# Optimization experiments

Measured on AMD Instinct MI355X. Metric: run time of the kernel, lower is better.

Reference implementation:

```python
import jax, jax.numpy as jnp
import numpy as np

D_MODEL = 1024
N_HEADS = 16
D_HEAD = D_MODEL // N_HEADS


def setup_inputs() -> dict:
    key = jax.random.key(0)
    k1, k2, k3, k4, k5 = jax.random.split(key, 5)
    B, S = 2, 2048
    scale_in = 1.0 / np.sqrt(D_MODEL)
    return {
        "x": jax.random.normal(k1, (B, S, D_MODEL), dtype=jnp.float32),
        "qkv_w": jax.random.normal(k2, (3 * D_MODEL, D_MODEL), dtype=jnp.float32) * scale_in,
        "qkv_b": jax.random.normal(k3, (3 * D_MODEL,), dtype=jnp.float32) * 0.02,
        "out_w": jax.random.normal(k4, (D_MODEL, D_MODEL), dtype=jnp.float32) * scale_in,
        "out_b": jax.random.normal(k5, (D_MODEL,), dtype=jnp.float32) * 0.02,
    }


def reference(x, qkv_w, qkv_b, out_w, out_b) -> jnp.ndarray:
    B, S, D = x.shape
    # qkv projection: torch Linear stores weight as (out, in)
    qkv = x @ qkv_w.T + qkv_b                      # [B,S,3D]
    qkv = qkv.reshape(B, S, 3, N_HEADS, D_HEAD)
    qkv = jnp.transpose(qkv, (2, 0, 3, 1, 4))      # [3,B,H,S,d]
    q, k, v = qkv[0], qkv[1], qkv[2]
    scale = 1.0 / np.sqrt(D_HEAD).astype(np.float32)
    scores = jnp.einsum("bhsd,bhtd->bhst", q, k) * scale  # [B,H,S,S]
    attn = jax.nn.softmax(scores, axis=-1)
    out = jnp.einsum("bhst,bhtd->bhsd", attn, v)   # [B,H,S,d]
    out = jnp.transpose(out, (0, 2, 1, 3)).reshape(B, S, D)
    return out @ out_w.T + out_b
```

## Files before the change

### kernel.cpp

```cpp
#include <hip/hip_runtime.h>

typedef __bf16 bf16;
typedef __bf16 bf16x4 __attribute__((ext_vector_type(4)));
typedef __bf16 bf16x8 __attribute__((ext_vector_type(8)));
typedef float  f32x4  __attribute__((ext_vector_type(4)));

__device__ __forceinline__ void gld16(const void* g, void* l) {
  __builtin_amdgcn_global_load_lds(
      (const __attribute__((address_space(1))) void*)g,
      (__attribute__((address_space(3))) void*)l, 16, 0, 0);
}

__global__ void f2bf4_kernel(const float* __restrict__ in, bf16* __restrict__ out, int n4) {
  int i = blockIdx.x * blockDim.x + threadIdx.x;
  if (i < n4) {
    float4 v = reinterpret_cast<const float4*>(in)[i];
    bf16x4 o = { (bf16)v.x, (bf16)v.y, (bf16)v.z, (bf16)v.w };
    reinterpret_cast<bf16x4*>(out)[i] = o;
  }
}

template<int MODE>
__global__ __launch_bounds__(256)
void gemm_bt(const bf16* __restrict__ A, const bf16* __restrict__ B,
             const float* __restrict__ bias, void* __restrict__ Cout,
             int K, int N) {
  __shared__ bf16 As[128 * 64];
  __shared__ bf16 Bs[128 * 64];
  const int tid  = threadIdx.x;
  const int wave = tid >> 6, lane = tid & 63;
  const int quad = lane >> 4, l16 = lane & 15;
  const int bm = blockIdx.x * 128, bn = blockIdx.y * 128;
  const int wr = (wave >> 1) * 64, wc = (wave & 1) * 64;
  const int arow = lane >> 3;
  const int acol = (lane & 7) * 8;

  f32x4 acc[4][4] = {};

  const bf16* Ab = A + (size_t)bm * K;
  const bf16* Bb = B + (size_t)bn * K;

  for (int k0 = 0; k0 < K; k0 += 64) {
#pragma unroll
    for (int i = 0; i < 4; ++i) {
      int c = wave * 4 + i;
      gld16(Ab + (size_t)(c * 8 + arow) * K + k0 + acol, As + c * 512);
      gld16(Bb + (size_t)(c * 8 + arow) * K + k0 + acol, Bs + c * 512);
    }
    __syncthreads();
#pragma unroll
    for (int kk = 0; kk < 64; kk += 32) {
      bf16x8 af[4], bfr[4];
#pragma unroll
      for (int i = 0; i < 4; ++i)
        af[i]  = *(const bf16x8*)(As + (wr + i * 16 + l16) * 64 + kk + quad * 8);
#pragma unroll
      for (int i = 0; i < 4; ++i)
        bfr[i] = *(const bf16x8*)(Bs + (wc + i * 16 + l16) * 64 + kk + quad * 8);
#pragma unroll
      for (int i = 0; i < 4; ++i)
#pragma unroll
        for (int j = 0; j < 4; ++j)
          acc[i][j] = __builtin_amdgcn_mfma_f32_16x16x32_bf16(af[i], bfr[j], acc[i][j], 0, 0, 0);
    }
    __syncthreads();
  }

  if constexpr (MODE == 0) {
    bf16* Q = (bf16*)Cout;
#pragma unroll
    for (int j = 0; j < 4; ++j) {
      int col = bn + wc + j * 16 + l16;
      float bv  = bias[col];
      int sec = col >> 10, rem = col & 1023;
      int h = rem >> 6, d = rem & 63;
      float scl = (sec == 0) ? 0.125f * 1.44269504f : 1.0f;
#pragma unroll
      for (int i = 0; i < 4; ++i) {
#pragma unroll
        for (int r = 0; r < 4; ++r) {
          int row = bm + wr + i * 16 + quad * 4 + r;
          int b = row >> 11, si = row & 2047;
          float v = (acc[i][j][r] + bv) * scl;
          Q[(((size_t)sec * 32 + b * 16 + h) * 2048 + si) * 64 + d] = (bf16)v;
        }
      }
    }
  } else {
    float* C = (float*)Cout;
#pragma unroll
    for (int j = 0; j < 4; ++j) {
      int col = bn + wc + j * 16 + l16;
      float bv = bias[col];
#pragma unroll
      for (int i = 0; i < 4; ++i)
#pragma unroll
        for (int r = 0; r < 4; ++r) {
          int row = bm + wr + i * 16 + quad * 4 + r;
          C[(size_t)row * N + col] = acc[i][j][r] + bv;
        }
    }
  }
}

__global__ __launch_bounds__(256)
void transpose_v(const bf16* __restrict__ V, bf16* __restrict__ Vt) {
  __shared__ bf16 t[64][72];
  int bh = blockIdx.y, s0 = blockIdx.x * 64;
  const bf16* Vb = V + ((size_t)bh * 2048 + s0) * 64;
  bf16* Vtb = Vt + (size_t)bh * 64 * 2048 + s0;
  int tid = threadIdx.x;
#pragma unroll
  for (int p = 0; p < 2; ++p) {
    int r = p * 32 + (tid >> 3), c0 = (tid & 7) * 8;
    bf16x8 v = *(const bf16x8*)(Vb + r * 64 + c0);
#pragma unroll
    for (int j = 0; j < 8; ++j) t[c0 + j][r] = v[j];
  }
  __syncthreads();
#pragma unroll
  for (int p = 0; p < 2; ++p) {
    int d = p * 32 + (tid >> 3), s = (tid & 7) * 8;
    *(bf16x8*)(Vtb + (size_t)d * 2048 + s) = *(const bf16x8*)(&t[d][s]);
  }
}

__global__ __launch_bounds__(256, 2)
void attn_kernel(const bf16* __restrict__ QKV, const bf16* __restrict__ Vt,
                 bf16* __restrict__ O) {
  __shared__ bf16 Qs[128 * 72];
  __shared__ bf16 Ks[128 * 72];
  __shared__ bf16 Ps[4][32 * 144];

  const int bh = blockIdx.y;
  const int q0 = blockIdx.x * 128;
  const bf16* Qg = QKV + ((size_t)bh * 2048 + q0) * 64;
  const bf16* Kg = QKV + (size_t)32 * 2048 * 64 + (size_t)bh * 2048 * 64;
  const bf16* Vg = Vt + (size_t)bh * 64 * 2048;

  const int tid  = threadIdx.x;
  const int wave = tid >> 6, lane = tid & 63;
  const int quad = lane >> 4, l16 = lane & 15;
  const int srow = tid >> 3;
  const int scol = (tid & 7) * 8;

#pragma unroll
  for (int ch = 0; ch < 4; ++ch) {
    int row = ch * 32 + srow;
    *(bf16x8*)(Qs + row * 72 + scol) = *(const bf16x8*)(Qg + row * 64 + scol);
  }

  float rs[2][4] = {};
  f32x4 o[2][4] = {};

  for (int kt = 0; kt < 16; ++kt) {
    bf16x8 kreg[4];
#pragma unroll
    for (int ch = 0; ch < 4; ++ch)
      kreg[ch] = *(const bf16x8*)(Kg + (size_t)(kt * 128 + ch * 32 + srow) * 64 + scol);

    bf16x8 bv[4][4];
#pragma unroll
    for (int kk = 0; kk < 4; ++kk)
#pragma unroll
      for (int oj = 0; oj < 4; ++oj)
        bv[kk][oj] = *(const bf16x8*)(Vg + (size_t)(oj * 16 + l16) * 2048 +
                                      kt * 128 + kk * 32 + quad * 8);

    __syncthreads();
#pragma unroll
    for (int ch = 0; ch < 4; ++ch)
      *(bf16x8*)(Ks + (ch * 32 + srow) * 72 + scol) = kreg[ch];
    __syncthreads();

    f32x4 s[2][8] = {};
#pragma unroll
    for (int kk = 0; kk < 64; kk += 32) {
      bf16x8 aq0 = *(const bf16x8*)(Qs + (wave * 32 + l16) * 72 + kk + quad * 8);
      bf16x8 aq1 = *(const bf16x8*)(Qs + (wave * 32 + 16 + l16) * 72 + kk + quad * 8);
#pragma unroll
      for (int ni = 0; ni < 8; ++ni) {
        bf16x8 bk = *(const bf16x8*)(Ks + (ni * 16 + l16) * 72 + kk + quad * 8);
        s[0][ni] = __builtin_amdgcn_mfma_f32_16x16x32_bf16(aq0, bk, s[0][ni], 0, 0, 0);
        s[1][ni] = __builtin_amdgcn_mfma_f32_16x16x32_bf16(aq1, bk, s[1][ni], 0, 0, 0);
      }
    }

#pragma unroll
    for (int i = 0; i < 2; ++i)
#pragma unroll
      for (int ni = 0; ni < 8; ++ni)
#pragma unroll
        for (int r = 0; r < 4; ++r) {
          float p = __builtin_amdgcn_exp2f(s[i][ni][r]);
          rs[i][r] += p;
          Ps[wave][(i * 16 + quad * 4 + r) * 144 + ni * 16 + l16] = (bf16)p;
        }

#pragma unroll
    for (int kk = 0; kk < 4; ++kk) {
#pragma unroll
      for (int i = 0; i < 2; ++i) {
        bf16x8 ap = *(const bf16x8*)(&Ps[wave][(i * 16 + l16) * 144 + kk * 32 + quad * 8]);
#pragma unroll
        for (int oj = 0; oj < 4; ++oj)
          o[i][oj] = __builtin_amdgcn_mfma_f32_16x16x32_bf16(ap, bv[kk][oj], o[i][oj], 0, 0, 0);
      }
    }
  }

#pragma unroll
  for (int i = 0; i < 2; ++i)
#pragma unroll
    for (int r = 0; r < 4; ++r) {
#pragma unroll
      for (int d = 1; d < 16; d <<= 1) rs[i][r] += __shfl_xor(rs[i][r], d);
    }

  const int b = bh >> 4, h = bh & 15;
#pragma unroll
  for (int i = 0; i < 2; ++i)
#pragma unroll
    for (int r = 0; r < 4; ++r) {
      float inv = 1.0f / rs[i][r];
      int row = q0 + wave * 32 + i * 16 + quad * 4 + r;
#pragma unroll
      for (int oj = 0; oj < 4; ++oj)
        O[((size_t)(b * 2048 + row)) * 1024 + h * 64 + oj * 16 + l16] =
            (bf16)(o[i][oj][r] * inv);
    }
}

extern "C" void kernel_launch(void* const* d_in, const int* in_sizes, int n_in,
                              void* d_out, int out_size, void* d_ws, size_t ws_size,
                              hipStream_t stream) {
  const float* x      = (const float*)d_in[0];
  const float* qkv_w  = (const float*)d_in[1];
  const float* qkv_b  = (const float*)d_in[2];
  const float* out_w  = (const float*)d_in[3];
  const float* out_b  = (const float*)d_in[4];
  float* out = (float*)d_out;

  char* ws = (char*)d_ws;
  bf16* Xb   = (bf16*)(ws);
  bf16* Wqkv = (bf16*)(ws + 8388608);
  bf16* Wout = (bf16*)(ws + 14680064);
  bf16* QKV  = (bf16*)(ws + 16777216);
  bf16* At   = (bf16*)(ws + 41943040);
  bf16* Vt   = Xb;

  f2bf4_kernel<<<4096, 256, 0, stream>>>(x,     Xb,   1048576);
  f2bf4_kernel<<<3072, 256, 0, stream>>>(qkv_w, Wqkv, 786432);
  f2bf4_kernel<<<1024, 256, 0, stream>>>(out_w, Wout, 262144);

  gemm_bt<0><<<dim3(32, 24), 256, 0, stream>>>(Xb, Wqkv, qkv_b, (void*)QKV, 1024, 3072);

  transpose_v<<<dim3(32, 32), 256, 0, stream>>>(QKV + (size_t)2 * 32 * 2048 * 64, Vt);

  attn_kernel<<<dim3(16, 32), 256, 0, stream>>>(QKV, Vt, At);

  gemm_bt<1><<<dim3(32, 8), 256, 0, stream>>>(At, Wout, out_b, (void*)out, 1024, 1024);
}
```

Before: 231.7 us.

## Double-buffer K in attention, keep Q in registers, fuse casts, retile out-proj GEMM

The attention kernel now holds Q fragments in registers and double-buffers K tiles in LDS, prefetching the next tile while the current one computes, so each iteration needs one barrier instead of two. It also swaps MFMA operand order so P is stored as packed 4-wide writes with a smaller padded stride, and the row-sum shuffle reduction is shorter. The three fp32-to-bf16 casts are merged into one launch, and the output projection uses 128x64 tiles so it runs twice as many blocks. The cost is extra LDS and register pressure, and the transposed S layout has to stay consistent with the P read-back.

```diff
diff --git a/kernel.cpp b/kernel.cpp
--- a/kernel.cpp
+++ b/kernel.cpp
@@ -11,31 +11,38 @@
       (__attribute__((address_space(3))) void*)l, 16, 0, 0);
 }
 
-__global__ void f2bf4_kernel(const float* __restrict__ in, bf16* __restrict__ out, int n4) {
+__global__ void f2bf_all(const float* __restrict__ x, bf16* __restrict__ xo,
+                         const float* __restrict__ w1, bf16* __restrict__ w1o,
+                         const float* __restrict__ w2, bf16* __restrict__ w2o) {
   int i = blockIdx.x * blockDim.x + threadIdx.x;
-  if (i < n4) {
-    float4 v = reinterpret_cast<const float4*>(in)[i];
-    bf16x4 o = { (bf16)v.x, (bf16)v.y, (bf16)v.z, (bf16)v.w };
-    reinterpret_cast<bf16x4*>(out)[i] = o;
-  }
-}
-
-template<int MODE>
+  const float* in; bf16* out; int idx;
+  if (i < 1048576)      { in = x;  out = xo;  idx = i; }
+  else if (i < 1835008) { in = w1; out = w1o; idx = i - 1048576; }
+  else                  { in = w2; out = w2o; idx = i - 1835008; }
+  float4 v = reinterpret_cast<const float4*>(in)[idx];
+  bf16x4 o = { (bf16)v.x, (bf16)v.y, (bf16)v.z, (bf16)v.w };
+  reinterpret_cast<bf16x4*>(out)[idx] = o;
+}
+
+template<int MODE, int BN>
 __global__ __launch_bounds__(256)
 void gemm_bt(const bf16* __restrict__ A, const bf16* __restrict__ B,
              const float* __restrict__ bias, void* __restrict__ Cout,
              int K, int N) {
   __shared__ bf16 As[128 * 64];
-  __shared__ bf16 Bs[128 * 64];
+  __shared__ bf16 Bs[BN * 64];
   const int tid  = threadIdx.x;
   const int wave = tid >> 6, lane = tid & 63;
   const int quad = lane >> 4, l16 = lane & 15;
-  const int bm = blockIdx.x * 128, bn = blockIdx.y * 128;
-  const int wr = (wave >> 1) * 64, wc = (wave & 1) * 64;
+  const int bm = blockIdx.x * 128, bn = blockIdx.y * BN;
+  constexpr int NI  = (BN == 128) ? 4 : 2;
+  constexpr int BCH = BN / 32;
+  const int wr = (BN == 128) ? (wave >> 1) * 64 : wave * 32;
+  const int wc = (BN == 128) ? (wave & 1) * 64 : 0;
   const int arow = lane >> 3;
   const int acol = (lane & 7) * 8;
 
-  f32x4 acc[4][4] = {};
+  f32x4 acc[NI][4] = {};
 
   const bf16* Ab = A + (size_t)bm * K;
   const bf16* Bb = B + (size_t)bn * K;
@@ -45,20 +52,24 @@
     for (int i = 0; i < 4; ++i) {
       int c = wave * 4 + i;
       gld16(Ab + (size_t)(c * 8 + arow) * K + k0 + acol, As + c * 512);
+    }
+#pragma unroll
+    for (int i = 0; i < BCH; ++i) {
+      int c = wave * BCH + i;
       gld16(Bb + (size_t)(c * 8 + arow) * K + k0 + acol, Bs + c * 512);
     }
     __syncthreads();
 #pragma unroll
     for (int kk = 0; kk < 64; kk += 32) {
-      bf16x8 af[4], bfr[4];
-#pragma unroll
-      for (int i = 0; i < 4; ++i)
+      bf16x8 af[NI], bfr[4];
+#pragma unroll
+      for (int i = 0; i < NI; ++i)
         af[i]  = *(const bf16x8*)(As + (wr + i * 16 + l16) * 64 + kk + quad * 8);
 #pragma unroll
-      for (int i = 0; i < 4; ++i)
-        bfr[i] = *(const bf16x8*)(Bs + (wc + i * 16 + l16) * 64 + kk + quad * 8);
-#pragma unroll
-      for (int i = 0; i < 4; ++i)
+      for (int j = 0; j < 4; ++j)
+        bfr[j] = *(const bf16x8*)(Bs + (wc + j * 16 + l16) * 64 + kk + quad * 8);
+#pragma unroll
+      for (int i = 0; i < NI; ++i)
 #pragma unroll
         for (int j = 0; j < 4; ++j)
           acc[i][j] = __builtin_amdgcn_mfma_f32_16x16x32_bf16(af[i], bfr[j], acc[i][j], 0, 0, 0);
@@ -76,7 +87,7 @@
       int h = rem >> 6, d = rem & 63;
       float scl = (sec == 0) ? 0.125f * 1.44269504f : 1.0f;
 #pragma unroll
-      for (int i = 0; i < 4; ++i) {
+      for (int i = 0; i < NI; ++i) {
 #pragma unroll
         for (int r = 0; r < 4; ++r) {
           int row = bm + wr + i * 16 + quad * 4 + r;
@@ -93,7 +104,7 @@
       int col = bn + wc + j * 16 + l16;
       float bv = bias[col];
 #pragma unroll
-      for (int i = 0; i < 4; ++i)
+      for (int i = 0; i < NI; ++i)
 #pragma unroll
         for (int r = 0; r < 4; ++r) {
           int row = bm + wr + i * 16 + quad * 4 + r;
@@ -128,9 +139,8 @@
 __global__ __launch_bounds__(256, 2)
 void attn_kernel(const bf16* __restrict__ QKV, const bf16* __restrict__ Vt,
                  bf16* __restrict__ O) {
-  __shared__ bf16 Qs[128 * 72];
-  __shared__ bf16 Ks[128 * 72];
-  __shared__ bf16 Ps[4][32 * 144];
+  __shared__ bf16 Ks[2][128 * 72];
+  __shared__ bf16 Ps[4][32 * 136];
 
   const int bh = blockIdx.y;
   const int q0 = blockIdx.x * 128;
@@ -143,22 +153,39 @@
   const int quad = lane >> 4, l16 = lane & 15;
   const int srow = tid >> 3;
   const int scol = (tid & 7) * 8;
-
-#pragma unroll
-  for (int ch = 0; ch < 4; ++ch) {
-    int row = ch * 32 + srow;
-    *(bf16x8*)(Qs + row * 72 + scol) = *(const bf16x8*)(Qg + row * 64 + scol);
-  }
-
-  float rs[2][4] = {};
+  bf16* Pw = &Ps[wave][0];
+
+  bf16x8 aq[2][2];
+#pragma unroll
+  for (int i = 0; i < 2; ++i)
+#pragma unroll
+    for (int kh = 0; kh < 2; ++kh)
+      aq[i][kh] = *(const bf16x8*)(Qg + (size_t)(wave * 32 + i * 16 + l16) * 64 +
+                                   kh * 32 + quad * 8);
+
+  {
+    bf16x8 kreg[4];
+#pragma unroll
+    for (int ch = 0; ch < 4; ++ch)
+      kreg[ch] = *(const bf16x8*)(Kg + (size_t)(ch * 32 + srow) * 64 + scol);
+#pragma unroll
+    for (int ch = 0; ch < 4; ++ch)
+      *(bf16x8*)(&Ks[0][(ch * 32 + srow) * 72 + scol]) = kreg[ch];
+  }
+  __syncthreads();
+
+  float rs[2] = {0.f, 0.f};
   f32x4 o[2][4] = {};
 
   for (int kt = 0; kt < 16; ++kt) {
+    const int cur = kt & 1;
+
     bf16x8 kreg[4];
-#pragma unroll
-    for (int ch = 0; ch < 4; ++ch)
-      kreg[ch] = *(const bf16x8*)(Kg + (size_t)(kt * 128 + ch * 32 + srow) * 64 + scol);
-
+    if (kt < 15) {
+#pragma unroll
+      for (int ch = 0; ch < 4; ++ch)
+        kreg[ch] = *(const bf16x8*)(Kg + (size_t)((kt + 1) * 128 + ch * 32 + srow) * 64 + scol);
+    }
     bf16x8 bv[4][4];
 #pragma unroll
     for (int kk = 0; kk < 4; ++kk)
@@ -167,62 +194,63 @@
         bv[kk][oj] = *(const bf16x8*)(Vg + (size_t)(oj * 16 + l16) * 2048 +
                                       kt * 128 + kk * 32 + quad * 8);
 
-    __syncthreads();
-#pragma unroll
-    for (int ch = 0; ch < 4; ++ch)
-      *(bf16x8*)(Ks + (ch * 32 + srow) * 72 + scol) = kreg[ch];
-    __syncthreads();
-
     f32x4 s[2][8] = {};
 #pragma unroll
-    for (int kk = 0; kk < 64; kk += 32) {
-      bf16x8 aq0 = *(const bf16x8*)(Qs + (wave * 32 + l16) * 72 + kk + quad * 8);
-      bf16x8 aq1 = *(const bf16x8*)(Qs + (wave * 32 + 16 + l16) * 72 + kk + quad * 8);
+    for (int kh = 0; kh < 2; ++kh) {
 #pragma unroll
       for (int ni = 0; ni < 8; ++ni) {
-        bf16x8 bk = *(const bf16x8*)(Ks + (ni * 16 + l16) * 72 + kk + quad * 8);
-        s[0][ni] = __builtin_amdgcn_mfma_f32_16x16x32_bf16(aq0, bk, s[0][ni], 0, 0, 0);
-        s[1][ni] = __builtin_amdgcn_mfma_f32_16x16x32_bf16(aq1, bk, s[1][ni], 0, 0, 0);
-      }
+        bf16x8 bk = *(const bf16x8*)(&Ks[cur][(ni * 16 + l16) * 72 + kh * 32 + quad * 8]);
+        s[0][ni] = __builtin_amdgcn_mfma_f32_16x16x32_bf16(bk, aq[0][kh], s[0][ni], 0, 0, 0);
+        s[1][ni] = __builtin_amdgcn_mfma_f32_16x16x32_bf16(bk, aq[1][kh], s[1][ni], 0, 0, 0);
+      }
+    }
+
+    if (kt < 15) {
+#pragma unroll
+      for (int ch = 0; ch < 4; ++ch)
+        *(bf16x8*)(&Ks[cur ^ 1][(ch * 32 + srow) * 72 + scol]) = kreg[ch];
     }
 
 #pragma unroll
     for (int i = 0; i < 2; ++i)
 #pragma unroll
-      for (int ni = 0; ni < 8; ++ni)
-#pragma unroll
-        for (int r = 0; r < 4; ++r) {
-          float p = __builtin_amdgcn_exp2f(s[i][ni][r]);
-          rs[i][r] += p;
-          Ps[wave][(i * 16 + quad * 4 + r) * 144 + ni * 16 + l16] = (bf16)p;
-        }
+      for (int ni = 0; ni < 8; ++ni) {
+        float p0 = __builtin_amdgcn_exp2f(s[i][ni][0]);
+        float p1 = __builtin_amdgcn_exp2f(s[i][ni][1]);
+        float p2 = __builtin_amdgcn_exp2f(s[i][ni][2]);
+        float p3 = __builtin_amdgcn_exp2f(s[i][ni][3]);
+        rs[i] += (p0 + p1) + (p2 + p3);
+        bf16x4 pk = { (bf16)p0, (bf16)p1, (bf16)p2, (bf16)p3 };
+        *(bf16x4*)(Pw + (i * 16 + l16) * 136 + ni * 16 + quad * 4) = pk;
+      }
 
 #pragma unroll
     for (int kk = 0; kk < 4; ++kk) {
 #pragma unroll
       for (int i = 0; i < 2; ++i) {
-        bf16x8 ap = *(const bf16x8*)(&Ps[wave][(i * 16 + l16) * 144 + kk * 32 + quad * 8]);
+        bf16x8 ap = *(const bf16x8*)(Pw + (i * 16 + l16) * 136 + kk * 32 + quad * 8);
 #pragma unroll
         for (int oj = 0; oj < 4; ++oj)
           o[i][oj] = __builtin_amdgcn_mfma_f32_16x16x32_bf16(ap, bv[kk][oj], o[i][oj], 0, 0, 0);
       }
     }
-  }
-
+
+    __syncthreads();
+  }
+
+#pragma unroll
+  for (int i = 0; i < 2; ++i) {
+    rs[i] += __shfl_xor(rs[i], 16);
+    rs[i] += __shfl_xor(rs[i], 32);
+  }
+
+  const int b = bh >> 4, h = bh & 15;
 #pragma unroll
   for (int i = 0; i < 2; ++i)
 #pragma unroll
     for (int r = 0; r < 4; ++r) {
-#pragma unroll
-      for (int d = 1; d < 16; d <<= 1) rs[i][r] += __shfl_xor(rs[i][r], d);
-    }
-
-  const int b = bh >> 4, h = bh & 15;
-#pragma unroll
-  for (int i = 0; i < 2; ++i)
-#pragma unroll
-    for (int r = 0; r < 4; ++r) {
-      float inv = 1.0f / rs[i][r];
+      float lsum = __shfl(rs[i], quad * 4 + r);
+      float inv = 1.0f / lsum;
       int row = q0 + wave * 32 + i * 16 + quad * 4 + r;
 #pragma unroll
       for (int oj = 0; oj < 4; ++oj)
@@ -249,15 +277,13 @@
   bf16* At   = (bf16*)(ws + 41943040);
   bf16* Vt   = Xb;
 
-  f2bf4_kernel<<<4096, 256, 0, stream>>>(x,     Xb,   1048576);
-  f2bf4_kernel<<<3072, 256, 0, stream>>>(qkv_w, Wqkv, 786432);
-  f2bf4_kernel<<<1024, 256, 0, stream>>>(out_w, Wout, 262144);
-
-  gemm_bt<0><<<dim3(32, 24), 256, 0, stream>>>(Xb, Wqkv, qkv_b, (void*)QKV, 1024, 3072);
+  f2bf_all<<<8192, 256, 0, stream>>>(x, Xb, qkv_w, Wqkv, out_w, Wout);
+
+  gemm_bt<0, 128><<<dim3(32, 24), 256, 0, stream>>>(Xb, Wqkv, qkv_b, (void*)QKV, 1024, 3072);
 
   transpose_v<<<dim3(32, 32), 256, 0, stream>>>(QKV + (size_t)2 * 32 * 2048 * 64, Vt);
 
   attn_kernel<<<dim3(16, 32), 256, 0, stream>>>(QKV, Vt, At);
 
-  gemm_bt<1><<<dim3(32, 8), 256, 0, stream>>>(At, Wout, out_b, (void*)out, 1024, 1024);
-}
+  gemm_bt<1, 64><<<dim3(32, 16), 256, 0, stream>>>(At, Wout, out_b, (void*)out, 1024, 1024);
+}
```

New measurement: 228.1 us. Within noise of the previous version (-1.6%).
